# Optimization experiments

Measured on AMD Instinct MI355X. Metric: run time of the kernel, lower is better.

Reference implementation:

```python
import jax, jax.numpy as jnp
import numpy as np

BN_EPS = 1e-5


def setup_inputs() -> dict:
    key = jax.random.key(0)
    ks = jax.random.split(key, 12)
    B, C, L, P = 8, 128, 4096, 96
    d = C // 8
    return {
        "x": jax.random.normal(ks[0], (B, C, 1), jnp.float32),
        "Wt": jax.random.normal(ks[1], (C, C, L), jnp.float32) * 0.02,
        "bt": jax.random.normal(ks[2], (C,), jnp.float32) * 0.02,
        "gamma": jnp.ones((C,), jnp.float32),
        "beta": jnp.zeros((C,), jnp.float32),
        "Wq": jax.random.normal(ks[3], (d, C), jnp.float32) * 0.05,
        "bq": jax.random.normal(ks[4], (d,), jnp.float32) * 0.02,
        "Wk": jax.random.normal(ks[5], (d, C), jnp.float32) * 0.05,
        "bk": jax.random.normal(ks[6], (d,), jnp.float32) * 0.02,
        "Wv": jax.random.normal(ks[7], (C, C), jnp.float32) * 0.05,
        "bv": jax.random.normal(ks[8], (C,), jnp.float32) * 0.02,
        "W2": jax.random.normal(ks[9], (P, C), jnp.float32) * 0.05,
        "b2": jax.random.normal(ks[10], (P,), jnp.float32) * 0.02,
    }


def reference(x, Wt, bt, gamma, beta, Wq, bq, Wk, bk, Wv, bv, W2, b2):
    # l1: ConvTranspose1d(C, C, kernel=L, stride=1) on input of length 1
    # out[b, o, l] = sum_i x[b, i, 0] * Wt[i, o, l] + bt[o]
    h = jnp.einsum('bi,iol->bol', x[:, :, 0], Wt) + bt[None, :, None]  # [B,C,L]
    # BatchNorm1d (training mode: batch stats, biased variance)
    mean = jnp.mean(h, axis=(0, 2), keepdims=True)
    var = jnp.mean((h - mean) ** 2, axis=(0, 2), keepdims=True)
    h = (h - mean) * jax.lax.rsqrt(var + BN_EPS)
    h = h * gamma[None, :, None] + beta[None, :, None]
    h = jax.nn.relu(h)
    # Self_Attn: 1x1 conv projections
    q = jnp.einsum('qc,bcl->bql', Wq, h) + bq[None, :, None]   # [B,d,L]
    k = jnp.einsum('qc,bcl->bql', Wk, h) + bk[None, :, None]   # [B,d,L]
    v = jnp.einsum('oc,bcl->bol', Wv, h) + bv[None, :, None]   # [B,C,L]
    energy = jnp.einsum('bdl,bdm->blm', q, k)                  # [B,L,L]
    attn = jax.nn.softmax(energy, axis=-1)
    out = jnp.einsum('bcm,blm->bcl', v, attn)                  # [B,C,L]
    # l2: Conv1d(C -> P, kernel=1)
    y = jnp.einsum('pc,bcl->bpl', W2, out) + b2[None, :, None]  # [B,P,L]
    return y
```

## Files before the change

kernel.cpp:

```cpp
#include <hip/hip_runtime.h>

#define B_ 8
#define C_ 128
#define L_ 4096
#define P_ 96
#define D_ 16

typedef __attribute__((ext_vector_type(8))) short short8;
typedef __attribute__((ext_vector_type(16))) float float16v;

__device__ __forceinline__ unsigned short f2bf(float f) {
  unsigned int u = __float_as_uint(f);
  u += 0x7fff + ((u >> 16) & 1);
  return (unsigned short)(u >> 16);
}

constexpr size_t OFF_H      = 0;
constexpr size_t OFF_PSUM   = 16777216;
constexpr size_t OFF_PSUMSQ = OFF_PSUM + 8192;
constexpr size_t OFF_SCALE  = OFF_PSUMSQ + 8192;
constexpr size_t OFF_SHIFT  = OFF_SCALE + 512;
constexpr size_t OFF_WALLT  = OFF_SHIFT + 512;
constexpr size_t OFF_BALL   = OFF_WALLT + 65536;
constexpr size_t OFF_QT     = OFF_BALL + 512;
constexpr size_t OFF_KT     = OFF_QT + 1048576;
constexpr size_t OFF_V2     = OFF_KT + 1048576;

__global__ __launch_bounds__(128) void k_prep(
    const float* __restrict__ Wq, const float* __restrict__ bq,
    const float* __restrict__ Wk, const float* __restrict__ bk,
    const float* __restrict__ Wv, const float* __restrict__ bv,
    const float* __restrict__ W2,
    float* __restrict__ wallT, float* __restrict__ ball)
{
  const int r = blockIdx.x;
  const int c = threadIdx.x;
  float wv;
  if (r < 16) {
    wv = Wq[r * C_ + c];
  } else if (r < 32) {
    wv = Wk[(r - 16) * C_ + c];
  } else {
    const int p = r - 32;
    float s = 0.f;
#pragma unroll 8
    for (int o = 0; o < C_; ++o) s += W2[p * C_ + o] * Wv[o * C_ + c];
    wv = s;
  }
  wallT[c * C_ + r] = wv;
  if (c == 0) {
    float bb;
    if (r < 16)      bb = bq[r];
    else if (r < 32) bb = bk[r - 16];
    else {
      const int p = r - 32;
      float s = 0.f;
#pragma unroll 8
      for (int o = 0; o < C_; ++o) s += W2[p * C_ + o] * bv[o];
      bb = s;
    }
    ball[r] = bb;
  }
}

__global__ __launch_bounds__(256) void k_conv(
    const float* __restrict__ x, const float* __restrict__ Wt,
    float* __restrict__ h, float* __restrict__ psum, float* __restrict__ psumsq)
{
  __shared__ float4 xs4[256];
  __shared__ float rs1[4], rs2[4];
  const int tid = threadIdx.x;
  const int o = blockIdx.y;
  const int l = blockIdx.x * 1024 + tid * 4;

  xs4[tid] = ((const float4*)x)[tid];
  __syncthreads();

  float4 acc[8];
#pragma unroll
  for (int bb = 0; bb < 8; ++bb) acc[bb] = (float4){0.f, 0.f, 0.f, 0.f};

  const float* wp = Wt + (size_t)o * L_ + l;
  const size_t stride = (size_t)C_ * L_;
  const int phase = (blockIdx.y + blockIdx.x * 8) & 31;

  float4 wbuf[2][4];
#pragma unroll
  for (int q = 0; q < 4; ++q)
    wbuf[0][q] = *(const float4*)(wp + (size_t)(phase * 4 + q) * stride);

#pragma unroll 2
  for (int g = 0; g < 32; ++g) {
    const int cur = g & 1, nb = cur ^ 1;
    const int in4 = ((phase + g + 1) & 31) * 4;
#pragma unroll
    for (int q = 0; q < 4; ++q)
      wbuf[nb][q] = *(const float4*)(wp + (size_t)(in4 + q) * stride);

    const int ic = (phase + g) & 31;
#pragma unroll
    for (int bb = 0; bb < 8; ++bb) {
      const float4 xb = xs4[bb * 32 + ic];
      acc[bb].x += xb.x * wbuf[cur][0].x + xb.y * wbuf[cur][1].x + xb.z * wbuf[cur][2].x + xb.w * wbuf[cur][3].x;
      acc[bb].y += xb.x * wbuf[cur][0].y + xb.y * wbuf[cur][1].y + xb.z * wbuf[cur][2].y + xb.w * wbuf[cur][3].y;
      acc[bb].z += xb.x * wbuf[cur][0].z + xb.y * wbuf[cur][1].z + xb.z * wbuf[cur][2].z + xb.w * wbuf[cur][3].z;
      acc[bb].w += xb.x * wbuf[cur][0].w + xb.y * wbuf[cur][1].w + xb.z * wbuf[cur][2].w + xb.w * wbuf[cur][3].w;
    }
  }
  float s1 = 0.f, s2 = 0.f;
#pragma unroll
  for (int bb = 0; bb < 8; ++bb) {
    *(float4*)(h + ((size_t)(bb * C_ + o)) * L_ + l) = acc[bb];
    s1 += acc[bb].x + acc[bb].y + acc[bb].z + acc[bb].w;
    s2 += acc[bb].x * acc[bb].x + acc[bb].y * acc[bb].y
        + acc[bb].z * acc[bb].z + acc[bb].w * acc[bb].w;
  }
  for (int off = 1; off < 64; off <<= 1) {
    s1 += __shfl_xor(s1, off);
    s2 += __shfl_xor(s2, off);
  }
  if ((tid & 63) == 0) { rs1[tid >> 6] = s1; rs2[tid >> 6] = s2; }
  __syncthreads();
  if (tid == 0) {
    psum[o * 4 + blockIdx.x]   = rs1[0] + rs1[1] + rs1[2] + rs1[3];
    psumsq[o * 4 + blockIdx.x] = rs2[0] + rs2[1] + rs2[2] + rs2[3];
  }
}

__global__ __launch_bounds__(128) void k_bn(
    const float* __restrict__ psum, const float* __restrict__ psumsq,
    const float* __restrict__ gamma, const float* __restrict__ beta,
    float* __restrict__ scale, float* __restrict__ shift)
{
  const int c = threadIdx.x;
  float s1 = 0.f, s2 = 0.f;
  for (int t = 0; t < 4; ++t) { s1 += psum[c * 4 + t]; s2 += psumsq[c * 4 + t]; }
  const float inv = 1.f / 32768.f;
  const float mean = s1 * inv;
  const float var  = s2 * inv - mean * mean;
  const float sc   = rsqrtf(var + 1e-5f) * gamma[c];
  scale[c] = sc;
  shift[c] = beta[c] - mean * sc;
}

__global__ __launch_bounds__(256) void k_proj(
    const float* __restrict__ h, const float* __restrict__ scale,
    const float* __restrict__ shift, const float* __restrict__ wallT,
    const float* __restrict__ ball,
    unsigned short* __restrict__ qT, unsigned short* __restrict__ kT,
    unsigned short* __restrict__ v2t)
{
  __shared__ __align__(16) char sm[128 * 68 * 4];
  float* hn = (float*)sm;
  unsigned short* v2s = (unsigned short*)sm;

  const int b = blockIdx.y;
  const int l0 = blockIdx.x * 64;
  const int tid = threadIdx.x;

#pragma unroll
  for (int i = 0; i < 8; ++i) {
    const int idx = tid + i * 256;
    const int c = idx >> 4, lq = (idx & 15) * 4;
    const float4 hv = *(const float4*)(h + ((size_t)(b * C_ + c)) * L_ + l0 + lq);
    const float sc = scale[c], sh = shift[c];
    float4 r;
    r.x = fmaxf(hv.x * sc + sh, 0.f);
    r.y = fmaxf(hv.y * sc + sh, 0.f);
    r.z = fmaxf(hv.z * sc + sh, 0.f);
    r.w = fmaxf(hv.w * sc + sh, 0.f);
    *(float4*)(hn + c * 68 + lq) = r;
  }
  __syncthreads();

  const int wu = __builtin_amdgcn_readfirstlane(tid) >> 6;
  const int lane = tid & 63;
  const int l = l0 + lane;

  float acc[32];
#pragma unroll
  for (int r = 0; r < 32; ++r) acc[r] = ball[wu * 32 + r];

#pragma unroll 4
  for (int c = 0; c < C_; ++c) {
    const float hv = hn[c * 68 + lane];
    const float* wrow = wallT + c * C_ + wu * 32;
#pragma unroll
    for (int r = 0; r < 32; ++r) acc[r] += wrow[r] * hv;
  }
  __syncthreads();

  if (wu == 0) {
    const size_t row = (size_t)(b * L_ + l) * D_;
    short8 v0, v1;
#pragma unroll
    for (int r = 0; r < 8; ++r) {
      v0[r] = (short)f2bf(acc[r] * 1.44269504f);
      v1[r] = (short)f2bf(acc[8 + r] * 1.44269504f);
    }
    *(short8*)(qT + row) = v0;  *(short8*)(qT + row + 8) = v1;
#pragma unroll
    for (int r = 0; r < 8; ++r) { v0[r] = (short)f2bf(acc[16 + r]); v1[r] = (short)f2bf(acc[24 + r]); }
    *(short8*)(kT + row) = v0;  *(short8*)(kT + row + 8) = v1;
  } else {
    const int pbase = wu * 32 - 32;
#pragma unroll
    for (int r = 0; r < 32; ++r)
      v2s[(pbase + r) * 72 + lane] = f2bf(acc[r]);
  }
  __syncthreads();

#pragma unroll
  for (int i = 0; i < 6; ++i) {
    const int j = tid + i * 256;
    const int mo4 = j & 3;
    const int jp = j >> 2;
    const int p = jp % 96;
    const int mtl = jp / 96;
    const uint2 val = *(const uint2*)(v2s + p * 72 + mtl * 16 + mo4 * 4);
    *(uint2*)(v2t + ((size_t)((b * (L_ / 16) + blockIdx.x * 4 + mtl)) * P_ + p) * 16
              + mo4 * 4) = val;
  }
}

__global__ __launch_bounds__(1024, 4) void k_attn(
    const unsigned short* __restrict__ qT, const unsigned short* __restrict__ kT,
    const unsigned short* __restrict__ v2t, const float* __restrict__ b2,
    float* __restrict__ y)
{
  __shared__ float ldsO[P_ * 128];
  __shared__ float ldsL[128];

  const int b = blockIdx.y;
  const int l0 = blockIdx.x * 128;
  const int tid = threadIdx.x;
  const int w  = tid >> 6;
  const int qg = w & 3;
  const int ms = w >> 2;
  const int lane = tid & 63;
  const int col = lane & 31;
  const int hh  = lane >> 5;

#pragma unroll
  for (int i = 0; i < 12; ++i) ldsO[tid + i * 1024] = 0.f;
  if (tid < 128) ldsL[tid] = 0.f;
  __syncthreads();

  const int lq = l0 + qg * 32 + col;
  const short8 qf = *(const short8*)(qT + ((size_t)(b * L_ + lq)) * D_ + hh * 8);

  float16v oacc[3];
#pragma unroll
  for (int pt = 0; pt < 3; ++pt)
#pragma unroll
    for (int r = 0; r < 16; ++r) oacc[pt][r] = 0.f;
  float lsum = 0.f;

  const unsigned short* kbase =
      kT + ((size_t)(b * L_ + ms * 1024 + col)) * D_ + hh * 8;
  const unsigned short* vtb = v2t + (size_t)b * (L_ / 16) * P_ * 16
                              + (size_t)col * 16 + hh * 8;

  short8 kf_cur = *(const short8*)(kbase);

#pragma unroll 2
  for (int it = 0; it < 32; ++it) {
    const int itn = (it + 1) & 31;
    const short8 kf_nxt = *(const short8*)(kbase + (size_t)itn * 32 * D_);

    const int mt16 = ms * 64 + it * 2;
    short8 vf[6];
#pragma unroll
    for (int mt = 0; mt < 2; ++mt)
#pragma unroll
      for (int pt = 0; pt < 3; ++pt)
        vf[mt * 3 + pt] = *(const short8*)(vtb
            + ((size_t)(mt16 + mt) * P_ + pt * 32) * 16);

    float16v zero;
#pragma unroll
    for (int r = 0; r < 16; ++r) zero[r] = 0.f;
    const float16v s = __builtin_amdgcn_mfma_f32_32x32x16_bf16(kf_cur, qf, zero, 0, 0, 0);

    unsigned dw[8];
#pragma unroll
    for (int g = 0; g < 8; ++g) {
      const float e0 = __builtin_amdgcn_exp2f(s[2 * g]);
      const float e1 = __builtin_amdgcn_exp2f(s[2 * g + 1]);
      lsum += e0 + e1;
      const unsigned u0 = __float_as_uint(e0) + 0x8000u;
      const unsigned u1 = __float_as_uint(e1) + 0x8000u;
      dw[g] = __builtin_amdgcn_perm(u1, u0, 0x07060302u);
    }

#pragma unroll
    for (int mt = 0; mt < 2; ++mt) {
      const unsigned t0 = hh ? dw[4 * mt + 0] : dw[4 * mt + 2];
      const unsigned t1 = hh ? dw[4 * mt + 1] : dw[4 * mt + 3];
      const unsigned r0 = (unsigned)__shfl_xor((int)t0, 32);
      const unsigned r1 = (unsigned)__shfl_xor((int)t1, 32);
      union { int4 i; short8 s8; } pu;
      pu.i.x = hh ? (int)r0 : (int)dw[4 * mt + 0];
      pu.i.y = hh ? (int)r1 : (int)dw[4 * mt + 1];
      pu.i.z = hh ? (int)dw[4 * mt + 2] : (int)r0;
      pu.i.w = hh ? (int)dw[4 * mt + 3] : (int)r1;
      const short8 pf = pu.s8;
#pragma unroll
      for (int pt = 0; pt < 3; ++pt)
        oacc[pt] = __builtin_amdgcn_mfma_f32_32x32x16_bf16(vf[mt * 3 + pt], pf, oacc[pt], 0, 0, 0);
    }
    kf_cur = kf_nxt;
  }

  atomicAdd(&ldsL[qg * 32 + col], lsum);
#pragma unroll
  for (int pt = 0; pt < 3; ++pt)
#pragma unroll
    for (int r = 0; r < 16; ++r) {
      const int p = (r & 3) + 8 * (r >> 2) + 4 * hh + 32 * pt;
      atomicAdd(&ldsO[p * 128 + qg * 32 + col], oacc[pt][r]);
    }
  __syncthreads();

#pragma unroll
  for (int i = 0; i < 12; ++i) {
    const int idx = tid + i * 1024;
    const int p = idx >> 7;
    const int l = idx & 127;
    y[((size_t)(b * P_ + p)) * L_ + l0 + l] = ldsO[idx] / ldsL[l] + b2[p];
  }
}

extern "C" void kernel_launch(void* const* d_in, const int* in_sizes, int n_in,
                              void* d_out, int out_size, void* d_ws, size_t ws_size,
                              hipStream_t stream) {
  (void)in_sizes; (void)n_in; (void)out_size; (void)ws_size;
  const float* x     = (const float*)d_in[0];
  const float* Wt    = (const float*)d_in[1];
  const float* gamma = (const float*)d_in[3];
  const float* beta  = (const float*)d_in[4];
  const float* Wq    = (const float*)d_in[5];
  const float* bq    = (const float*)d_in[6];
  const float* Wk    = (const float*)d_in[7];
  const float* bk    = (const float*)d_in[8];
  const float* Wv    = (const float*)d_in[9];
  const float* bv    = (const float*)d_in[10];
  const float* W2    = (const float*)d_in[11];
  const float* b2    = (const float*)d_in[12];
  float* y = (float*)d_out;

  char* ws = (char*)d_ws;
  float* h       = (float*)(ws + OFF_H);
  float* psum    = (float*)(ws + OFF_PSUM);
  float* psumsq  = (float*)(ws + OFF_PSUMSQ);
  float* scale   = (float*)(ws + OFF_SCALE);
  float* shift   = (float*)(ws + OFF_SHIFT);
  float* wallT   = (float*)(ws + OFF_WALLT);
  float* ball    = (float*)(ws + OFF_BALL);
  unsigned short* qT  = (unsigned short*)(ws + OFF_QT);
  unsigned short* kT  = (unsigned short*)(ws + OFF_KT);
  unsigned short* v2t = (unsigned short*)(ws + OFF_V2);

  k_prep<<<128, 128, 0, stream>>>(Wq, bq, Wk, bk, Wv, bv, W2, wallT, ball);
  k_conv<<<dim3(4, 128), 256, 0, stream>>>(x, Wt, h, psum, psumsq);
  k_bn<<<1, 128, 0, stream>>>(psum, psumsq, gamma, beta, scale, shift);
  k_proj<<<dim3(64, 8), 256, 0, stream>>>(h, scale, shift, wallT, ball, qT, kT, v2t);
  k_attn<<<dim3(32, 8), 1024, 0, stream>>>(qT, kT, v2t, b2, y);
}
```

Baseline: 525.4 us.

## Split attention key range across two blocks and add combine kernel

The attention kernel now splits the key dimension in half, giving twice as many blocks (512 instead of 256). Each block writes partial unnormalized outputs and row sums to workspace, and a new combine kernel adds the halves, normalizes and applies the bias. The conv kernel also moves to 128-thread blocks with twice the grid, and the BN partial-sum count rises to match. This targets low occupancy on a GPU with many CUs (256 blocks of 1024 threads), at the cost of about 25MB of extra partial-output traffic and one more launch.

Measured after the change: 1.342 ms. +155.5%, slower.

```diff
diff --git a/kernel.cpp b/kernel.cpp
--- a/kernel.cpp
+++ b/kernel.cpp
@@ -25,6 +25,8 @@
 constexpr size_t OFF_QT     = OFF_BALL + 512;
 constexpr size_t OFF_KT     = OFF_QT + 1048576;
 constexpr size_t OFF_V2     = OFF_KT + 1048576;
+constexpr size_t OFF_OP     = OFF_V2 + 6291456;
+constexpr size_t OFF_LP     = OFF_OP + 25165824;
 
 __global__ __launch_bounds__(128) void k_prep(
     const float* __restrict__ Wq, const float* __restrict__ bq,
@@ -43,7 +45,7 @@
   } else {
     const int p = r - 32;
     float s = 0.f;
-#pragma unroll 8
+#pragma unroll 16
     for (int o = 0; o < C_; ++o) s += W2[p * C_ + o] * Wv[o * C_ + c];
     wv = s;
   }
@@ -55,7 +57,7 @@
     else {
       const int p = r - 32;
       float s = 0.f;
-#pragma unroll 8
+#pragma unroll 16
       for (int o = 0; o < C_; ++o) s += W2[p * C_ + o] * bv[o];
       bb = s;
     }
@@ -63,17 +65,18 @@
   }
 }
 
-__global__ __launch_bounds__(256) void k_conv(
+__global__ __launch_bounds__(128) void k_conv(
     const float* __restrict__ x, const float* __restrict__ Wt,
     float* __restrict__ h, float* __restrict__ psum, float* __restrict__ psumsq)
 {
   __shared__ float4 xs4[256];
-  __shared__ float rs1[4], rs2[4];
+  __shared__ float rs1[2], rs2[2];
   const int tid = threadIdx.x;
   const int o = blockIdx.y;
-  const int l = blockIdx.x * 1024 + tid * 4;
+  const int l = blockIdx.x * 512 + tid * 4;
 
   xs4[tid] = ((const float4*)x)[tid];
+  xs4[tid + 128] = ((const float4*)x)[tid + 128];
   __syncthreads();
 
   float4 acc[8];
@@ -122,8 +125,8 @@
   if ((tid & 63) == 0) { rs1[tid >> 6] = s1; rs2[tid >> 6] = s2; }
   __syncthreads();
   if (tid == 0) {
-    psum[o * 4 + blockIdx.x]   = rs1[0] + rs1[1] + rs1[2] + rs1[3];
-    psumsq[o * 4 + blockIdx.x] = rs2[0] + rs2[1] + rs2[2] + rs2[3];
+    psum[o * 8 + blockIdx.x]   = rs1[0] + rs1[1];
+    psumsq[o * 8 + blockIdx.x] = rs2[0] + rs2[1];
   }
 }
 
@@ -134,7 +137,7 @@
 {
   const int c = threadIdx.x;
   float s1 = 0.f, s2 = 0.f;
-  for (int t = 0; t < 4; ++t) { s1 += psum[c * 4 + t]; s2 += psumsq[c * 4 + t]; }
+  for (int t = 0; t < 8; ++t) { s1 += psum[c * 8 + t]; s2 += psumsq[c * 8 + t]; }
   const float inv = 1.f / 32768.f;
   const float mean = s1 * inv;
   const float var  = s2 * inv - mean * mean;
@@ -223,15 +226,17 @@
   }
 }
 
-__global__ __launch_bounds__(1024, 4) void k_attn(
+__global__ __launch_bounds__(1024, 8) void k_attn(
     const unsigned short* __restrict__ qT, const unsigned short* __restrict__ kT,
-    const unsigned short* __restrict__ v2t, const float* __restrict__ b2,
-    float* __restrict__ y)
+    const unsigned short* __restrict__ v2t,
+    float* __restrict__ OP, float* __restrict__ LP)
 {
   __shared__ float ldsO[P_ * 128];
   __shared__ float ldsL[128];
 
-  const int b = blockIdx.y;
+  const int bidx = blockIdx.y;
+  const int b = bidx >> 1;
+  const int half = bidx & 1;
   const int l0 = blockIdx.x * 128;
   const int tid = threadIdx.x;
   const int w  = tid >> 6;
@@ -241,11 +246,6 @@
   const int col = lane & 31;
   const int hh  = lane >> 5;
 
-#pragma unroll
-  for (int i = 0; i < 12; ++i) ldsO[tid + i * 1024] = 0.f;
-  if (tid < 128) ldsL[tid] = 0.f;
-  __syncthreads();
-
   const int lq = l0 + qg * 32 + col;
   const short8 qf = *(const short8*)(qT + ((size_t)(b * L_ + lq)) * D_ + hh * 8);
 
@@ -256,19 +256,21 @@
     for (int r = 0; r < 16; ++r) oacc[pt][r] = 0.f;
   float lsum = 0.f;
 
+  const int mbase0 = half * 2048 + ms * 512;
   const unsigned short* kbase =
-      kT + ((size_t)(b * L_ + ms * 1024 + col)) * D_ + hh * 8;
+      kT + ((size_t)(b * L_ + mbase0 + col)) * D_ + hh * 8;
   const unsigned short* vtb = v2t + (size_t)b * (L_ / 16) * P_ * 16
                               + (size_t)col * 16 + hh * 8;
+  const int t16base = mbase0 >> 4;
 
   short8 kf_cur = *(const short8*)(kbase);
 
 #pragma unroll 2
-  for (int it = 0; it < 32; ++it) {
-    const int itn = (it + 1) & 31;
+  for (int it = 0; it < 16; ++it) {
+    const int itn = (it + 1) & 15;
     const short8 kf_nxt = *(const short8*)(kbase + (size_t)itn * 32 * D_);
 
-    const int mt16 = ms * 64 + it * 2;
+    const int mt16 = t16base + it * 2;
     short8 vf[6];
 #pragma unroll
     for (int mt = 0; mt < 2; ++mt)
@@ -312,6 +314,11 @@
     kf_cur = kf_nxt;
   }
 
+#pragma unroll
+  for (int i = 0; i < 12; ++i) ldsO[tid + i * 1024] = 0.f;
+  if (tid < 128) ldsL[tid] = 0.f;
+  __syncthreads();
+
   atomicAdd(&ldsL[qg * 32 + col], lsum);
 #pragma unroll
   for (int pt = 0; pt < 3; ++pt)
@@ -322,12 +329,41 @@
     }
   __syncthreads();
 
+  const size_t slot = (size_t)bidx * 32 + blockIdx.x;
+  float* opb = OP + slot * (P_ * 128);
+#pragma unroll
+  for (int i = 0; i < 12; ++i) opb[tid + i * 1024] = ldsO[tid + i * 1024];
+  if (tid < 128) LP[slot * 128 + tid] = ldsL[tid];
+}
+
+__global__ __launch_bounds__(256) void k_comb(
+    const float* __restrict__ OP, const float* __restrict__ LP,
+    const float* __restrict__ b2, float* __restrict__ y)
+{
+  __shared__ float linv[128];
+  const int lt = blockIdx.x, b = blockIdx.y;
+  const int s0 = (b * 2 + 0) * 32 + lt;
+  const int s1 = (b * 2 + 1) * 32 + lt;
+  const int tid = threadIdx.x;
+  if (tid < 128)
+    linv[tid] = 1.f / (LP[s0 * 128 + tid] + LP[s1 * 128 + tid]);
+  __syncthreads();
+  const float4* a4 = (const float4*)(OP + (size_t)s0 * (P_ * 128));
+  const float4* c4 = (const float4*)(OP + (size_t)s1 * (P_ * 128));
 #pragma unroll
   for (int i = 0; i < 12; ++i) {
-    const int idx = tid + i * 1024;
-    const int p = idx >> 7;
-    const int l = idx & 127;
-    y[((size_t)(b * P_ + p)) * L_ + l0 + l] = ldsO[idx] / ldsL[l] + b2[p];
+    const int j = tid + i * 256;
+    const float4 a = a4[j];
+    const float4 c = c4[j];
+    const int p = j >> 5;
+    const int le = (j & 31) * 4;
+    const float bb = b2[p];
+    float4 o;
+    o.x = (a.x + c.x) * linv[le + 0] + bb;
+    o.y = (a.y + c.y) * linv[le + 1] + bb;
+    o.z = (a.z + c.z) * linv[le + 2] + bb;
+    o.w = (a.w + c.w) * linv[le + 3] + bb;
+    *(float4*)(y + ((size_t)(b * P_ + p)) * L_ + lt * 128 + le) = o;
   }
 }
 
@@ -360,10 +396,13 @@
   unsigned short* qT  = (unsigned short*)(ws + OFF_QT);
   unsigned short* kT  = (unsigned short*)(ws + OFF_KT);
   unsigned short* v2t = (unsigned short*)(ws + OFF_V2);
+  float* OP      = (float*)(ws + OFF_OP);
+  float* LP      = (float*)(ws + OFF_LP);
 
   k_prep<<<128, 128, 0, stream>>>(Wq, bq, Wk, bk, Wv, bv, W2, wallT, ball);
-  k_conv<<<dim3(4, 128), 256, 0, stream>>>(x, Wt, h, psum, psumsq);
+  k_conv<<<dim3(8, 128), 128, 0, stream>>>(x, Wt, h, psum, psumsq);
   k_bn<<<1, 128, 0, stream>>>(psum, psumsq, gamma, beta, scale, shift);
   k_proj<<<dim3(64, 8), 256, 0, stream>>>(h, scale, shift, wallT, ball, qT, kT, v2t);
-  k_attn<<<dim3(32, 8), 1024, 0, stream>>>(qT, kT, v2t, b2, y);
-}
+  k_attn<<<dim3(32, 16), 1024, 0, stream>>>(qT, kT, v2t, OP, LP);
+  k_comb<<<dim3(32, 8), 256, 0, stream>>>(OP, LP, b2, y);
+}
```
